# Optimization experiments

Measured on AMD Instinct MI355X. Metric: run time of the kernel, lower is better.

## Reference

```python
import jax, jax.numpy as jnp
import numpy as np

H, C = 8, 32          # heads, per-head channels (h_feats)
NEG_SLOPE = 0.2


def setup_inputs() -> dict:
    key = jax.random.key(0)
    ks = jax.random.split(key, 9)
    N, E, F_IN, F_E = 50000, 800000, 128, 16
    x = jax.random.normal(ks[0], (N, F_IN), jnp.float32)
    edge_index = jax.random.randint(ks[1], (2, E), 0, N, jnp.int64)
    edge_attr = jax.random.normal(ks[2], (E, F_E), jnp.float32)
    s = 1.0 / np.sqrt(F_IN)
    W = jax.random.normal(ks[3], (H * C, F_IN), jnp.float32) * s
    W_edge = jax.random.normal(ks[4], (H * C, F_E), jnp.float32) * (1.0 / np.sqrt(F_E))
    att_src = jax.random.normal(ks[5], (H, C), jnp.float32) * (1.0 / np.sqrt(C))
    att_dst = jax.random.normal(ks[6], (H, C), jnp.float32) * (1.0 / np.sqrt(C))
    att_edge = jax.random.normal(ks[7], (H, C), jnp.float32) * (1.0 / np.sqrt(C))
    bias = jnp.zeros((C,), jnp.float32)
    return {"x": x, "edge_index": edge_index, "edge_attr": edge_attr,
            "W": W, "W_edge": W_edge, "att_src": att_src, "att_dst": att_dst,
            "att_edge": att_edge, "bias": bias}


def reference(x, edge_index, edge_attr, W, W_edge, att_src, att_dst, att_edge, bias):
    N = x.shape[0]
    src, dst = edge_index[0], edge_index[1]

    # --- add self loops, edge_attr fill_value='mean' (per-dst mean of incoming attrs) ---
    deg = jax.ops.segment_sum(jnp.ones_like(dst, dtype=edge_attr.dtype), dst, num_segments=N)
    loop_attr = jax.ops.segment_sum(edge_attr, dst, num_segments=N) / jnp.maximum(deg, 1.0)[:, None]
    loop = jnp.arange(N, dtype=src.dtype)
    src = jnp.concatenate([src, loop])
    dst = jnp.concatenate([dst, loop])
    ea = jnp.concatenate([edge_attr, loop_attr], axis=0)  # [E+N, F_e]

    # --- node projection and per-node attention terms ---
    xh = (x @ W.T).reshape(N, H, C)                      # [N,H,C]
    a_src = jnp.einsum('nhc,hc->nh', xh, att_src)        # [N,H]
    a_dst = jnp.einsum('nhc,hc->nh', xh, att_dst)        # [N,H]

    # edge attention folded: (lin_edge(e).view(E,H,C) * att_edge).sum(-1) == e @ M
    M = jnp.einsum('hcf,hc->fh', W_edge.reshape(H, C, -1), att_edge)  # [F_e,H]
    a_edge = ea @ M                                      # [E+N,H]

    alpha = a_src[src] + a_dst[dst] + a_edge             # [E+N,H]
    alpha = jnp.where(alpha >= 0, alpha, NEG_SLOPE * alpha)

    # --- scatter-softmax over edges grouped by dst node ---
    amax = jax.ops.segment_max(alpha, dst, num_segments=N)  # every node has a self loop
    ex = jnp.exp(alpha - amax[dst])
    denom = jax.ops.segment_sum(ex, dst, num_segments=N)
    att = ex / denom[dst]                                # [E+N,H]

    # --- weighted message scatter-sum ---
    msg = xh[src] * att[..., None]                       # [E+N,H,C]
    out = jax.ops.segment_sum(msg, dst, num_segments=N)  # [N,H,C]
    return out.mean(axis=1) + bias                       # concat=False -> head mean
```

## Files before the change

kernel.cpp:

```cpp
#include <hip/hip_runtime.h>
#include <hip/hip_fp16.h>
#include <math.h>

#define H 8
#define C 32
#define HC 256
#define FE 16
#define FIN 128
#define NEG_SLOPE 0.2f

typedef __attribute__((ext_vector_type(8))) short bf16x8;
typedef __attribute__((ext_vector_type(4))) float f32x4;
typedef __attribute__((ext_vector_type(2))) float f32x2;

__device__ __forceinline__ unsigned short f2bf(float f) {
  unsigned int u = __float_as_uint(f);
  unsigned int lsb = (u >> 16) & 1u;
  u += 0x7fffu + lsb;
  return (unsigned short)(u >> 16);
}
__device__ __forceinline__ float bf2f(unsigned short s) {
  return __uint_as_float(((unsigned int)s) << 16);
}
__device__ __forceinline__ unsigned short f2h(float f) {
  return __half_as_ushort(__float2half(f));
}
__device__ __forceinline__ float h2f(unsigned short s) {
  return __half2float(__ushort_as_half(s));
}
__device__ __forceinline__ void pkfma(f32x2& acc, f32x2 x, f32x2 w) {
  asm volatile("v_pk_fma_f32 %0, %1, %2, %0" : "+v"(acc) : "v"(x), "v"(w));
}

__device__ __forceinline__ void split8(const float* v, bf16x8& hi, bf16x8& lo) {
#pragma unroll
  for (int i = 0; i < 8; ++i) {
    unsigned int u = __float_as_uint(v[i]);
    unsigned int hu = u & 0xffff0000u;
    float r = v[i] - __uint_as_float(hu);
    hi[i] = (short)(hu >> 16);
    lo[i] = (short)f2bf(r);
  }
}

__global__ __launch_bounds__(256) void k_xh(const float* __restrict__ x,
                                            const unsigned short* __restrict__ Whi,
                                            const unsigned short* __restrict__ Wlo,
                                            const float* __restrict__ att_src,
                                            const float* __restrict__ att_dst,
                                            unsigned short* __restrict__ xhb,
                                            float* __restrict__ a_dst,
                                            unsigned short* __restrict__ a_srch, int N) {
  int t = threadIdx.x;
  int w = t >> 6, lane = t & 63;
  int n15 = lane & 15, q = lane >> 4;
  int nodeBase = blockIdx.x * 128 + w * 32;
  int chBase = blockIdx.y * 128;

  f32x4 acc[8][2];
#pragma unroll
  for (int mt = 0; mt < 8; ++mt)
#pragma unroll
    for (int nt = 0; nt < 2; ++nt) acc[mt][nt] = (f32x4)(0.f);

  for (int ks = 0; ks < 4; ++ks) {
    int kOff = ks * 32 + q * 8;
    bf16x8 Bhi[2], Blo[2];
#pragma unroll
    for (int nt = 0; nt < 2; ++nt) {
      int node = nodeBase + nt * 16 + n15;
      int rn = (node < N) ? node : (N - 1);
      const float* px = &x[(size_t)rn * FIN + kOff];
      float vb[8];
      *(float4*)&vb[0] = *(const float4*)px;
      *(float4*)&vb[4] = *(const float4*)(px + 4);
      split8(vb, Bhi[nt], Blo[nt]);
    }
#pragma unroll
    for (int mt = 0; mt < 8; ++mt) {
      int widx = ((chBase + mt * 16 + n15) << 7) + kOff;
      bf16x8 Ahi = *(const bf16x8*)&Whi[widx];
      bf16x8 Alo = *(const bf16x8*)&Wlo[widx];
#pragma unroll
      for (int nt = 0; nt < 2; ++nt) {
        acc[mt][nt] = __builtin_amdgcn_mfma_f32_16x16x32_bf16(Ahi, Bhi[nt], acc[mt][nt], 0, 0, 0);
        acc[mt][nt] = __builtin_amdgcn_mfma_f32_16x16x32_bf16(Ahi, Blo[nt], acc[mt][nt], 0, 0, 0);
        acc[mt][nt] = __builtin_amdgcn_mfma_f32_16x16x32_bf16(Alo, Bhi[nt], acc[mt][nt], 0, 0, 0);
      }
    }
  }

  float ps[2][4] = {{0.f,0.f,0.f,0.f},{0.f,0.f,0.f,0.f}};
  float pd[2][4] = {{0.f,0.f,0.f,0.f},{0.f,0.f,0.f,0.f}};
#pragma unroll
  for (int mt = 0; mt < 8; ++mt) {
    int hl = mt >> 1;
#pragma unroll
    for (int r = 0; r < 4; ++r) {
      int ch = chBase + mt * 16 + q * 4 + r;
      float as_c = att_src[ch], ad_c = att_dst[ch];
#pragma unroll
      for (int nt = 0; nt < 2; ++nt) {
        float val = acc[mt][nt][r];
        ps[nt][hl] = fmaf(val, as_c, ps[nt][hl]);
        pd[nt][hl] = fmaf(val, ad_c, pd[nt][hl]);
      }
    }
#pragma unroll
    for (int nt = 0; nt < 2; ++nt) {
      int node = nodeBase + nt * 16 + n15;
      if (node < N) {
        ushort4 us;
        us.x = f2bf(acc[mt][nt][0]); us.y = f2bf(acc[mt][nt][1]);
        us.z = f2bf(acc[mt][nt][2]); us.w = f2bf(acc[mt][nt][3]);
        *(ushort4*)&xhb[(size_t)node * HC + chBase + mt * 16 + q * 4] = us;
      }
    }
  }
#pragma unroll
  for (int nt = 0; nt < 2; ++nt)
#pragma unroll
    for (int hl = 0; hl < 4; ++hl) {
      ps[nt][hl] += __shfl_xor(ps[nt][hl], 16, 64);
      ps[nt][hl] += __shfl_xor(ps[nt][hl], 32, 64);
      pd[nt][hl] += __shfl_xor(pd[nt][hl], 16, 64);
      pd[nt][hl] += __shfl_xor(pd[nt][hl], 32, 64);
    }
  if (q == 0) {
#pragma unroll
    for (int nt = 0; nt < 2; ++nt) {
      int node = nodeBase + nt * 16 + n15;
      if (node < N) {
        *(float4*)&a_dst[node * H + blockIdx.y * 4] = make_float4(pd[nt][0], pd[nt][1], pd[nt][2], pd[nt][3]);
        unsigned int p0 = (unsigned int)f2h(ps[nt][0]) | ((unsigned int)f2h(ps[nt][1]) << 16);
        unsigned int p1 = (unsigned int)f2h(ps[nt][2]) | ((unsigned int)f2h(ps[nt][3]) << 16);
        *(uint2*)&a_srch[(size_t)node * H + blockIdx.y * 4] = make_uint2(p0, p1);
      }
    }
  }
}

__global__ __launch_bounds__(256) void k_deg(const int* __restrict__ ei,
                                             int* __restrict__ deg,
                                             int* __restrict__ rank,
                                             const float* __restrict__ W,
                                             unsigned short* __restrict__ Whi,
                                             unsigned short* __restrict__ Wlo, int E) {
  int e = blockIdx.x * 256 + threadIdx.x;
  if (e < HC * FIN) {
    float v = W[e];
    unsigned int u = __float_as_uint(v);
    unsigned int hu = u & 0xffff0000u;
    Whi[e] = (unsigned short)(hu >> 16);
    Wlo[e] = f2bf(v - __uint_as_float(hu));
  }
  if (e < E) rank[e] = atomicAdd(&deg[ei[E + e]], 1);
}

__global__ __launch_bounds__(256) void k_scan(const int* __restrict__ deg,
                                              unsigned long long* __restrict__ st,
                                              int* __restrict__ rowptr, int N, int E) {
  __shared__ int buf[256];
  __shared__ int bofs_sh;
  int t = threadIdx.x, b = blockIdx.x;
  int i = b * 256 + t;
  int v = (i < N) ? deg[i] : 0;
  buf[t] = v;
  __syncthreads();
  for (int off = 1; off < 256; off <<= 1) {
    int y = (t >= off) ? buf[t - off] : 0;
    __syncthreads();
    buf[t] += y;
    __syncthreads();
  }
  if (t == 0) {
    int agg = buf[255];
    if (b == 0) {
      __hip_atomic_store(&st[0], (2ull << 32) | (unsigned int)agg, __ATOMIC_RELEASE, __HIP_MEMORY_SCOPE_AGENT);
      bofs_sh = 0;
    } else {
      __hip_atomic_store(&st[b], (1ull << 32) | (unsigned int)agg, __ATOMIC_RELEASE, __HIP_MEMORY_SCOPE_AGENT);
      int excl = 0;
      int p = b - 1;
      while (true) {
        unsigned long long s = __hip_atomic_load(&st[p], __ATOMIC_ACQUIRE, __HIP_MEMORY_SCOPE_AGENT);
        unsigned int flag = (unsigned int)(s >> 32);
        if (flag == 0u) { __builtin_amdgcn_s_sleep(1); continue; }
        excl += (int)(unsigned int)(s & 0xffffffffull);
        if (flag == 2u) break;
        --p;
      }
      __hip_atomic_store(&st[b], (2ull << 32) | (unsigned int)(excl + agg), __ATOMIC_RELEASE, __HIP_MEMORY_SCOPE_AGENT);
      bofs_sh = excl;
    }
  }
  __syncthreads();
  if (i < N) rowptr[i] = bofs_sh + buf[t] - v;
  if (i == 0) rowptr[N] = E;
}

__global__ __launch_bounds__(256) void k_edge_scatter(const int* __restrict__ ei,
                                                      const float* __restrict__ ea,
                                                      const float* __restrict__ W_edge,
                                                      const float* __restrict__ att_edge,
                                                      const unsigned short* __restrict__ a_srch,
                                                      const int* __restrict__ rowptr,
                                                      const int* __restrict__ rank,
                                                      unsigned int* __restrict__ recs,
                                                      int* __restrict__ sarr, int E) {
  __shared__ float Ms[FE * H];
  int t = threadIdx.x;
  if (t < FE * H) {
    int f = t >> 3, h = t & 7;
    float acc = 0.f;
#pragma unroll
    for (int c = 0; c < C; ++c)
      acc += W_edge[(h * C + c) * FE + f] * att_edge[h * C + c];
    Ms[f * H + h] = acc;
  }
  __syncthreads();
  int e0 = blockIdx.x * 512 + t;
  int e1 = e0 + 256;
  bool va = (e0 < E), vb = (e1 < E);
  int ca = va ? e0 : 0, cb = vb ? e1 : 0;
  int s0 = ei[ca], d0 = ei[E + ca];
  int s1 = ei[cb], d1 = ei[E + cb];
  const float4* pA = (const float4*)&ea[(size_t)ca * FE];
  const float4* pB = (const float4*)&ea[(size_t)cb * FE];
  float4 A0 = pA[0], A1 = pA[1], A2 = pA[2], A3 = pA[3];
  float4 B0 = pB[0], B1 = pB[1], B2 = pB[2], B3 = pB[3];
  int rk0 = rank[ca], rk1 = rank[cb];
  int rp0 = rowptr[d0], rp1 = rowptr[d1];
  uint4 asA = *(const uint4*)&a_srch[(size_t)s0 * H];
  uint4 asB = *(const uint4*)&a_srch[(size_t)s1 * H];

  float eavA[FE] = {A0.x, A0.y, A0.z, A0.w, A1.x, A1.y, A1.z, A1.w,
                    A2.x, A2.y, A2.z, A2.w, A3.x, A3.y, A3.z, A3.w};
  float eavB[FE] = {B0.x, B0.y, B0.z, B0.w, B1.x, B1.y, B1.z, B1.w,
                    B2.x, B2.y, B2.z, B2.w, B3.x, B3.y, B3.z, B3.w};
  float oA[H], oB[H];
#pragma unroll
  for (int h = 0; h < H; ++h) {
    float aa = 0.f, ab = 0.f;
#pragma unroll
    for (int f = 0; f < FE; ++f) {
      float m = Ms[f * H + h];
      aa += eavA[f] * m;
      ab += eavB[f] * m;
    }
    oA[h] = aa; oB[h] = ab;
  }
  unsigned int asw[2][4] = {{asA.x, asA.y, asA.z, asA.w}, {asB.x, asB.y, asB.z, asB.w}};
  if (va) {
    int pos = rp0 + rk0;
    unsigned int rec[H];
#pragma unroll
    for (int h = 0; h < H; ++h) {
      float asv = h2f((unsigned short)((h & 1) ? (asw[0][h >> 1] >> 16) : (asw[0][h >> 1] & 0xffffu)));
      rec[h] = (unsigned int)f2h(oA[h] + asv) | ((unsigned int)f2h(oA[h]) << 16);
    }
    uint4* rp = (uint4*)&recs[(size_t)pos * 8];
    rp[0] = make_uint4(rec[0], rec[1], rec[2], rec[3]);
    rp[1] = make_uint4(rec[4], rec[5], rec[6], rec[7]);
    sarr[pos] = s0;
  }
  if (vb) {
    int pos = rp1 + rk1;
    unsigned int rec[H];
#pragma unroll
    for (int h = 0; h < H; ++h) {
      float asv = h2f((unsigned short)((h & 1) ? (asw[1][h >> 1] >> 16) : (asw[1][h >> 1] & 0xffffu)));
      rec[h] = (unsigned int)f2h(oB[h] + asv) | ((unsigned int)f2h(oB[h]) << 16);
    }
    uint4* rp = (uint4*)&recs[(size_t)pos * 8];
    rp[0] = make_uint4(rec[0], rec[1], rec[2], rec[3]);
    rp[1] = make_uint4(rec[4], rec[5], rec[6], rec[7]);
    sarr[pos] = s1;
  }
}

__global__ __launch_bounds__(256) void k_node(const unsigned short* __restrict__ xhb,
                                              const unsigned short* __restrict__ a_srch,
                                              const float* __restrict__ a_dst,
                                              const unsigned int* __restrict__ recs,
                                              const int* __restrict__ sarr,
                                              const int* __restrict__ rowptr,
                                              const float* __restrict__ bias,
                                              float* __restrict__ out, int N) {
  __shared__ float wlds[4][512];
  __shared__ int   slds[4][64];
  int wv = threadIdx.x >> 6;
  int lane = threadIdx.x & 63;
  int n = blockIdx.x * 4 + wv;
  if (n >= N) return;
  int start = rowptr[n];
  int deg = rowptr[n + 1] - start;
  int jmax = (deg < 64) ? deg : 64;
  int nit = (jmax + 7) >> 3;
  int padded = nit << 3;
  int h = lane & 7, esub = lane >> 3;
  float adst = a_dst[n * H + h];
  float asrc = h2f(a_srch[(size_t)n * H + h]);

  if (lane < padded) slds[wv][lane] = (lane < jmax) ? sarr[start + lane] : n;

  const unsigned int* rb = recs + (size_t)start * 8 + lane;
  unsigned int u[8] = {0, 0, 0, 0, 0, 0, 0, 0};
#pragma unroll
  for (int it = 0; it < 8; ++it)
    if (it < nit) {
      int j = it * 8 + esub;
      if (j < jmax) u[it] = rb[it * 64];
    }

  int widx = ((esub >> 1) << 4) + (h << 1) + (esub & 1);
  float den = 0.f, psum = 0.f;
#pragma unroll
  for (int it = 0; it < 8; ++it)
    if (it < nit) {
      int j = it * 8 + esub;
      bool val = (j < jmax);
      float raw = h2f((unsigned short)(u[it] >> 16));
      float a = h2f((unsigned short)(u[it] & 0xffffu)) + adst;
      a = fmaxf(a, NEG_SLOPE * a);
      float w = val ? __expf(a) : 0.f;
      psum += val ? raw : 0.f;
      den += w;
      wlds[wv][it * 64 + widx] = w;
    }
  for (int j0 = 64; j0 < deg; j0 += 8) {
    int j = j0 + esub;
    if (j < deg) {
      unsigned int t2 = recs[(size_t)(start + j) * 8 + h];
      psum += h2f((unsigned short)(t2 >> 16));
      float a = h2f((unsigned short)(t2 & 0xffffu)) + adst;
      a = fmaxf(a, NEG_SLOPE * a);
      den += __expf(a);
    }
  }
#pragma unroll
  for (int m = 8; m <= 32; m <<= 1) {
    den += __shfl_xor(den, m, 64);
    psum += __shfl_xor(psum, m, 64);
  }
  float aself = asrc + adst + psum / fmaxf((float)deg, 1.f);
  aself = fmaxf(aself, NEG_SLOPE * aself);
  float wself = __expf(aself);
  float inv = 1.f / (den + wself);

  int hc = lane >> 3;
  float inv_c  = __shfl(inv, hc, 64);
  float ws_c   = __shfl(wself, hc, 64);
  float adst_c = __shfl(adst, hc, 64);
  f32x2 A0, A1, A2, A3;
  {
    uint2 su = ((const uint2*)(xhb + (((size_t)n) << 8)))[lane];
    A0[0] = ws_c * __uint_as_float(su.x << 16);         A0[1] = 0.f;
    A1[0] = ws_c * __uint_as_float(su.x & 0xffff0000u); A1[1] = 0.f;
    A2[0] = ws_c * __uint_as_float(su.y << 16);         A2[1] = 0.f;
    A3[0] = ws_c * __uint_as_float(su.y & 0xffff0000u); A3[1] = 0.f;
  }
  for (int j0 = 0; j0 < padded; j0 += 8) {
    uint2 v[8];
#pragma unroll
    for (int k = 0; k < 8; ++k)
      v[k] = ((const uint2*)(xhb + (((size_t)slds[wv][j0 + k]) << 8)))[lane];
#pragma unroll
    for (int k2 = 0; k2 < 4; ++k2) {
      f32x2 wp = *(const f32x2*)&wlds[wv][j0 * 8 + k2 * 16 + hc * 2];
      uint2 va = v[2 * k2], vb2 = v[2 * k2 + 1];
      f32x2 p;
      p[0] = __uint_as_float(va.x << 16);          p[1] = __uint_as_float(vb2.x << 16);
      pkfma(A0, p, wp);
      p[0] = __uint_as_float(va.x & 0xffff0000u);  p[1] = __uint_as_float(vb2.x & 0xffff0000u);
      pkfma(A1, p, wp);
      p[0] = __uint_as_float(va.y << 16);          p[1] = __uint_as_float(vb2.y << 16);
      pkfma(A2, p, wp);
      p[0] = __uint_as_float(va.y & 0xffff0000u);  p[1] = __uint_as_float(vb2.y & 0xffff0000u);
      pkfma(A3, p, wp);
    }
  }
  float accx = A0[0] + A0[1];
  float accy = A1[0] + A1[1];
  float accz = A2[0] + A2[1];
  float accw = A3[0] + A3[1];
  for (int j = 64; j < deg; ++j) {
    int src = sarr[start + j];
    unsigned int t2 = recs[(size_t)(start + j) * 8 + hc];
    float a = h2f((unsigned short)(t2 & 0xffffu)) + adst_c;
    a = fmaxf(a, NEG_SLOPE * a);
    float wj = __expf(a);
    uint2 v = ((const uint2*)(xhb + (((size_t)src) << 8)))[lane];
    accx = fmaf(__uint_as_float(v.x << 16), wj, accx);
    accy = fmaf(__uint_as_float(v.x & 0xffff0000u), wj, accy);
    accz = fmaf(__uint_as_float(v.y << 16), wj, accz);
    accw = fmaf(__uint_as_float(v.y & 0xffff0000u), wj, accw);
  }
  accx *= inv_c; accy *= inv_c; accz *= inv_c; accw *= inv_c;

#pragma unroll
  for (int m = 8; m <= 32; m <<= 1) {
    accx += __shfl_xor(accx, m, 64);
    accy += __shfl_xor(accy, m, 64);
    accz += __shfl_xor(accz, m, 64);
    accw += __shfl_xor(accw, m, 64);
  }
  if (lane < 8) {
    float4 b = ((const float4*)bias)[lane];
    float4 o;
    o.x = accx * 0.125f + b.x;
    o.y = accy * 0.125f + b.y;
    o.z = accz * 0.125f + b.z;
    o.w = accw * 0.125f + b.w;
    ((float4*)&out[(size_t)n * C])[lane] = o;
  }
}

extern "C" void kernel_launch(void* const* d_in, const int* in_sizes, int n_in,
                              void* d_out, int out_size, void* d_ws, size_t ws_size,
                              hipStream_t stream) {
  const float* x        = (const float*)d_in[0];
  const int*   ei       = (const int*)d_in[1];
  const float* ea       = (const float*)d_in[2];
  const float* W        = (const float*)d_in[3];
  const float* W_edge   = (const float*)d_in[4];
  const float* att_src  = (const float*)d_in[5];
  const float* att_dst  = (const float*)d_in[6];
  const float* att_edge = (const float*)d_in[7];
  const float* bias     = (const float*)d_in[8];
  float* out = (float*)d_out;

  int N = in_sizes[0] / FIN;
  int E = in_sizes[1] / 2;
  int nb = (N + 255) / 256;

  char* ws = (char*)d_ws;
  auto take = [&](size_t bytes) {
    char* p = ws;
    ws += (bytes + 255) & ~(size_t)255;
    return p;
  };
  unsigned short* xhb    = (unsigned short*)take((size_t)N * HC * 2);
  float*          a_dst  = (float*)take((size_t)N * H * 4);
  unsigned short* a_srch = (unsigned short*)take((size_t)N * H * 2);
  unsigned int*   recs   = (unsigned int*)take((size_t)E * 32);
  int*            sarr   = (int*)take((size_t)E * 4);
  unsigned short* Whi    = (unsigned short*)take((size_t)HC * FIN * 2);
  unsigned short* Wlo    = (unsigned short*)take((size_t)HC * FIN * 2);
  size_t degBytes = ((size_t)N * 4 + 7) & ~(size_t)7;
  char*  zbase    = take(degBytes + (size_t)nb * 8);
  int*            deg    = (int*)zbase;
  unsigned long long* st = (unsigned long long*)(zbase + degBytes);
  int*            rowptr = (int*)take((size_t)(N + 1) * 4);
  int*            rank   = (int*)take((size_t)E * 4);

  hipMemsetAsync(zbase, 0, degBytes + (size_t)nb * 8, stream);
  k_deg<<<(E + 255) / 256, 256, 0, stream>>>(ei, deg, rank, W, Whi, Wlo, E);
  k_xh<<<dim3((N + 127) / 128, 2), 256, 0, stream>>>(x, Whi, Wlo, att_src, att_dst, xhb, a_dst, a_srch, N);
  k_scan<<<nb, 256, 0, stream>>>(deg, st, rowptr, N, E);
  k_edge_scatter<<<(E + 511) / 512, 256, 0, stream>>>(ei, ea, W_edge, att_edge, a_srch, rowptr, rank, recs, sarr, E);
  k_node<<<(N + 3) / 4, 256, 0, stream>>>(xhb, a_srch, a_dst, recs, sarr, rowptr, bias, out, N);
}
```

Measured before the change: 330.8 us.

## Fuse degree counting with projection GEMM and replace decoupled-lookback scan

Merges the degree/rank atomic kernel and the node projection GEMM into a single launch, with block ranges split by index. The W hi/lo bf16 split is now done inline from fp32 W in each GEMM block instead of in a separate precompute pass. The single-pass decoupled-lookback scan is replaced by a two-kernel scan: per-block sums, then a second kernel that rescans block sums in shared memory. This removes launches and spin-waiting, at the cost of redundant W conversion work and one extra small kernel; it also relies on nb <= 256.

Result: faster. 299.6 us (-9.4%).

```diff
diff --git a/kernel.cpp b/kernel.cpp
--- a/kernel.cpp
+++ b/kernel.cpp
@@ -43,19 +43,31 @@
   }
 }
 
-__global__ __launch_bounds__(256) void k_xh(const float* __restrict__ x,
-                                            const unsigned short* __restrict__ Whi,
-                                            const unsigned short* __restrict__ Wlo,
-                                            const float* __restrict__ att_src,
-                                            const float* __restrict__ att_dst,
-                                            unsigned short* __restrict__ xhb,
-                                            float* __restrict__ a_dst,
-                                            unsigned short* __restrict__ a_srch, int N) {
+__global__ __launch_bounds__(256) void k_fused(const float* __restrict__ x,
+                                               const float* __restrict__ W,
+                                               const float* __restrict__ att_src,
+                                               const float* __restrict__ att_dst,
+                                               const int* __restrict__ ei,
+                                               int* __restrict__ deg,
+                                               int* __restrict__ rank,
+                                               unsigned short* __restrict__ xhb,
+                                               float* __restrict__ a_dst,
+                                               unsigned short* __restrict__ a_srch,
+                                               int N, int E, int nde, int nx) {
   int t = threadIdx.x;
+  if ((int)blockIdx.x < nde) {
+    int e = blockIdx.x * 256 + t;
+    if (e < E) rank[e] = atomicAdd(&deg[ei[E + e]], 1);
+    return;
+  }
+  int bb = blockIdx.x - nde;
+  int by = (bb >= nx) ? 1 : 0;
+  int bx = bb - by * nx;
+
   int w = t >> 6, lane = t & 63;
   int n15 = lane & 15, q = lane >> 4;
-  int nodeBase = blockIdx.x * 128 + w * 32;
-  int chBase = blockIdx.y * 128;
+  int nodeBase = bx * 128 + w * 32;
+  int chBase = by * 128;
 
   f32x4 acc[8][2];
 #pragma unroll
@@ -79,8 +91,12 @@
 #pragma unroll
     for (int mt = 0; mt < 8; ++mt) {
       int widx = ((chBase + mt * 16 + n15) << 7) + kOff;
-      bf16x8 Ahi = *(const bf16x8*)&Whi[widx];
-      bf16x8 Alo = *(const bf16x8*)&Wlo[widx];
+      const float* pw = &W[widx];
+      float wv8[8];
+      *(float4*)&wv8[0] = *(const float4*)pw;
+      *(float4*)&wv8[4] = *(const float4*)(pw + 4);
+      bf16x8 Ahi, Alo;
+      split8(wv8, Ahi, Alo);
 #pragma unroll
       for (int nt = 0; nt < 2; ++nt) {
         acc[mt][nt] = __builtin_amdgcn_mfma_f32_16x16x32_bf16(Ahi, Bhi[nt], acc[mt][nt], 0, 0, 0);
@@ -131,71 +147,49 @@
     for (int nt = 0; nt < 2; ++nt) {
       int node = nodeBase + nt * 16 + n15;
       if (node < N) {
-        *(float4*)&a_dst[node * H + blockIdx.y * 4] = make_float4(pd[nt][0], pd[nt][1], pd[nt][2], pd[nt][3]);
+        *(float4*)&a_dst[node * H + by * 4] = make_float4(pd[nt][0], pd[nt][1], pd[nt][2], pd[nt][3]);
         unsigned int p0 = (unsigned int)f2h(ps[nt][0]) | ((unsigned int)f2h(ps[nt][1]) << 16);
         unsigned int p1 = (unsigned int)f2h(ps[nt][2]) | ((unsigned int)f2h(ps[nt][3]) << 16);
-        *(uint2*)&a_srch[(size_t)node * H + blockIdx.y * 4] = make_uint2(p0, p1);
+        *(uint2*)&a_srch[(size_t)node * H + by * 4] = make_uint2(p0, p1);
       }
     }
   }
 }
 
-__global__ __launch_bounds__(256) void k_deg(const int* __restrict__ ei,
-                                             int* __restrict__ deg,
-                                             int* __restrict__ rank,
-                                             const float* __restrict__ W,
-                                             unsigned short* __restrict__ Whi,
-                                             unsigned short* __restrict__ Wlo, int E) {
-  int e = blockIdx.x * 256 + threadIdx.x;
-  if (e < HC * FIN) {
-    float v = W[e];
-    unsigned int u = __float_as_uint(v);
-    unsigned int hu = u & 0xffff0000u;
-    Whi[e] = (unsigned short)(hu >> 16);
-    Wlo[e] = f2bf(v - __uint_as_float(hu));
-  }
-  if (e < E) rank[e] = atomicAdd(&deg[ei[E + e]], 1);
-}
-
-__global__ __launch_bounds__(256) void k_scan(const int* __restrict__ deg,
-                                              unsigned long long* __restrict__ st,
-                                              int* __restrict__ rowptr, int N, int E) {
+__global__ __launch_bounds__(256) void k_scan1(const int* __restrict__ deg,
+                                               int* __restrict__ bsum, int N) {
+  int t = threadIdx.x;
+  int i = blockIdx.x * 256 + t;
+  int v = (i < N) ? deg[i] : 0;
+#pragma unroll
+  for (int m = 1; m < 64; m <<= 1) v += __shfl_xor(v, m, 64);
+  __shared__ int wsum[4];
+  if ((t & 63) == 0) wsum[t >> 6] = v;
+  __syncthreads();
+  if (t == 0) bsum[blockIdx.x] = wsum[0] + wsum[1] + wsum[2] + wsum[3];
+}
+
+__global__ __launch_bounds__(256) void k_scan23(const int* __restrict__ deg,
+                                                const int* __restrict__ bsum,
+                                                int* __restrict__ rowptr, int N, int E, int nb) {
+  __shared__ int sb[256];
   __shared__ int buf[256];
-  __shared__ int bofs_sh;
-  int t = threadIdx.x, b = blockIdx.x;
-  int i = b * 256 + t;
+  int t = threadIdx.x;
+  sb[t] = (t < nb) ? bsum[t] : 0;
+  int i = blockIdx.x * 256 + t;
   int v = (i < N) ? deg[i] : 0;
   buf[t] = v;
   __syncthreads();
   for (int off = 1; off < 256; off <<= 1) {
-    int y = (t >= off) ? buf[t - off] : 0;
+    int y1 = (t >= off) ? sb[t - off] : 0;
+    int y2 = (t >= off) ? buf[t - off] : 0;
     __syncthreads();
-    buf[t] += y;
+    sb[t] += y1;
+    buf[t] += y2;
     __syncthreads();
   }
-  if (t == 0) {
-    int agg = buf[255];
-    if (b == 0) {
-      __hip_atomic_store(&st[0], (2ull << 32) | (unsigned int)agg, __ATOMIC_RELEASE, __HIP_MEMORY_SCOPE_AGENT);
-      bofs_sh = 0;
-    } else {
-      __hip_atomic_store(&st[b], (1ull << 32) | (unsigned int)agg, __ATOMIC_RELEASE, __HIP_MEMORY_SCOPE_AGENT);
-      int excl = 0;
-      int p = b - 1;
-      while (true) {
-        unsigned long long s = __hip_atomic_load(&st[p], __ATOMIC_ACQUIRE, __HIP_MEMORY_SCOPE_AGENT);
-        unsigned int flag = (unsigned int)(s >> 32);
-        if (flag == 0u) { __builtin_amdgcn_s_sleep(1); continue; }
-        excl += (int)(unsigned int)(s & 0xffffffffull);
-        if (flag == 2u) break;
-        --p;
-      }
-      __hip_atomic_store(&st[b], (2ull << 32) | (unsigned int)(excl + agg), __ATOMIC_RELEASE, __HIP_MEMORY_SCOPE_AGENT);
-      bofs_sh = excl;
-    }
-  }
-  __syncthreads();
-  if (i < N) rowptr[i] = bofs_sh + buf[t] - v;
+  int bofs = (blockIdx.x == 0) ? 0 : sb[blockIdx.x - 1];
+  if (i < N) rowptr[i] = bofs + buf[t] - v;
   if (i == 0) rowptr[N] = E;
 }
 
@@ -433,6 +427,8 @@
   int N = in_sizes[0] / FIN;
   int E = in_sizes[1] / 2;
   int nb = (N + 255) / 256;
+  int nde = (E + 255) / 256;
+  int nx = (N + 127) / 128;
 
   char* ws = (char*)d_ws;
   auto take = [&](size_t bytes) {
@@ -445,19 +441,16 @@
   unsigned short* a_srch = (unsigned short*)take((size_t)N * H * 2);
   unsigned int*   recs   = (unsigned int*)take((size_t)E * 32);
   int*            sarr   = (int*)take((size_t)E * 4);
-  unsigned short* Whi    = (unsigned short*)take((size_t)HC * FIN * 2);
-  unsigned short* Wlo    = (unsigned short*)take((size_t)HC * FIN * 2);
-  size_t degBytes = ((size_t)N * 4 + 7) & ~(size_t)7;
-  char*  zbase    = take(degBytes + (size_t)nb * 8);
-  int*            deg    = (int*)zbase;
-  unsigned long long* st = (unsigned long long*)(zbase + degBytes);
+  int*            deg    = (int*)take((size_t)N * 4);
   int*            rowptr = (int*)take((size_t)(N + 1) * 4);
   int*            rank   = (int*)take((size_t)E * 4);
-
-  hipMemsetAsync(zbase, 0, degBytes + (size_t)nb * 8, stream);
-  k_deg<<<(E + 255) / 256, 256, 0, stream>>>(ei, deg, rank, W, Whi, Wlo, E);
-  k_xh<<<dim3((N + 127) / 128, 2), 256, 0, stream>>>(x, Whi, Wlo, att_src, att_dst, xhb, a_dst, a_srch, N);
-  k_scan<<<nb, 256, 0, stream>>>(deg, st, rowptr, N, E);
+  int*            bsum   = (int*)take((size_t)nb * 4);
+
+  hipMemsetAsync(deg, 0, (size_t)N * 4, stream);
+  k_fused<<<nde + 2 * nx, 256, 0, stream>>>(x, W, att_src, att_dst, ei, deg, rank,
+                                            xhb, a_dst, a_srch, N, E, nde, nx);
+  k_scan1<<<nb, 256, 0, stream>>>(deg, bsum, N);
+  k_scan23<<<nb, 256, 0, stream>>>(deg, bsum, rowptr, N, E, nb);
   k_edge_scatter<<<(E + 511) / 512, 256, 0, stream>>>(ei, ea, W_edge, att_edge, a_srch, rowptr, rank, recs, sarr, E);
   k_node<<<(N + 3) / 4, 256, 0, stream>>>(xhb, a_srch, a_dst, recs, sarr, rowptr, bias, out, N);
 }
```
